# Performance work log

Hardware: AMD Instinct MI355X
Metric: run time of the kernel (lower is better)

## Reference

```python
import jax, jax.numpy as jnp
import numpy as np

DECAY = 0.8
COMMITMENT = 1.0
EPS = 1e-05


def setup_inputs() -> dict:
    key = jax.random.key(0)
    k1, k2, k3 = jax.random.split(key, 3)
    dim, n_embed = 256, 8192
    input = jax.random.normal(k1, (8, 2048, dim), dtype=jnp.float32)
    embed = jax.random.normal(k2, (dim, n_embed), dtype=jnp.float32)
    cluster_size = jnp.zeros((n_embed,), dtype=jnp.float32)
    embed_avg = jax.random.normal(k3, (dim, n_embed), dtype=jnp.float32)
    return {"input": input, "embed": embed, "cluster_size": cluster_size, "embed_avg": embed_avg}


def reference(input, embed, cluster_size, embed_avg):
    dim, n_embed = embed.shape
    flatten = input.reshape(-1, dim)  # [N, d]
    dist = (jnp.sum(flatten * flatten, axis=1, keepdims=True)
            - 2.0 * flatten @ embed
            + jnp.sum(embed * embed, axis=0, keepdims=True))  # [N, C]
    embed_ind_flat = jnp.argmin(dist, axis=1)  # [N]
    embed_ind = embed_ind_flat.reshape(input.shape[:-1])
    quantize = jnp.take(embed.T, embed_ind_flat, axis=0).reshape(input.shape)

    # training-mode EMA codebook update (onehot.sum(0) and x^T @ onehot as segment ops)
    counts = jax.ops.segment_sum(jnp.ones_like(embed_ind_flat, dtype=input.dtype),
                                 embed_ind_flat, num_segments=n_embed)  # [C]
    embed_sum = jax.ops.segment_sum(flatten, embed_ind_flat, num_segments=n_embed).T  # [d, C]
    new_cluster_size = cluster_size * DECAY + counts * (1.0 - DECAY)
    new_embed_avg = embed_avg * DECAY + embed_sum * (1.0 - DECAY)
    smoothed = (new_cluster_size + EPS) / (jnp.sum(new_cluster_size) + n_embed * EPS)
    smoothed = smoothed * jnp.sum(new_cluster_size)
    new_embed = new_embed_avg / smoothed[None, :]

    commit_loss = jnp.mean((quantize - input) ** 2) * COMMITMENT
    # straight-through (no grad here in fwd-only, values identical)
    quantize_st = input + jax.lax.stop_gradient(quantize - input)
    return quantize_st, embed_ind, commit_loss, new_embed, new_cluster_size, new_embed_avg
```

## Files before the change

### kernel.cpp

```cpp
#include <hip/hip_runtime.h>
#include <hip/hip_bf16.h>
#include <float.h>
#include <stdint.h>

#define N_ROWS 16384
#define DIM 256
#define NE 8192
#define K2 768
#define DECAY 0.8f
#define OMD 0.2f
#define EPS 1e-5f
#define NPAN 8
#define NKT 24
#define NVT 96

#define WS_X2     0
#define WS_EMBEDT 0
#define WS_ESUMT  2097152
#define WS_B2T    6291456
#define WS_ENORM  9437184
#define WS_COUNTS 9445376
#define WS_SMOOTH 9453568
#define WS_PI     9592832
#define WS_LOSS   9740288
#define WS_TOTAL  9740289

#define OUT_Q    0
#define OUT_IND  4194304
#define OUT_LOSS 4210688
#define OUT_NE   4210689
#define OUT_NCS  6307841
#define OUT_NEA  6316033

typedef __attribute__((ext_vector_type(8))) short bf16x8;
typedef __attribute__((ext_vector_type(4))) float f32x4;

static __device__ __forceinline__ ushort f2bf(float f) {
    uint32_t u = __float_as_uint(f);
    uint32_t r = (u + 0x7fffu + ((u >> 16) & 1u)) >> 16;
    return (ushort)r;
}
static __device__ __forceinline__ float bf2f(ushort h) {
    return __uint_as_float(((uint32_t)h) << 16);
}
static __device__ __forceinline__ void async16(void* lds, const void* g) {
    __builtin_amdgcn_global_load_lds(
        (const __attribute__((address_space(1))) uint32_t*)g,
        (__attribute__((address_space(3))) uint32_t*)lds, 16, 0, 0);
}

__global__ __launch_bounds__(256) void convx_kernel(const float* __restrict__ x,
                                                    ushort* __restrict__ X2) {
    int i = blockIdx.x * 256 + threadIdx.x;
    int row = i >> 6, q = (i & 63) * 4;
    float4 v = *(const float4*)&x[(size_t)row * 256 + q];
    ushort4 hi, lo;
    hi.x = f2bf(v.x); hi.y = f2bf(v.y); hi.z = f2bf(v.z); hi.w = f2bf(v.w);
    lo.x = f2bf(v.x - bf2f(hi.x)); lo.y = f2bf(v.y - bf2f(hi.y));
    lo.z = f2bf(v.z - bf2f(hi.z)); lo.w = f2bf(v.w - bf2f(hi.w));
    *(ushort4*)&X2[(size_t)row * K2 + q]       = hi;
    *(ushort4*)&X2[(size_t)row * K2 + 256 + q] = lo;
    *(ushort4*)&X2[(size_t)row * K2 + 512 + q] = hi;
}

__global__ __launch_bounds__(256) void prepB_kernel(const float* __restrict__ embed,
                                                    ushort* __restrict__ B2T,
                                                    float* __restrict__ enorm) {
    __shared__ float t[32][33];
    int c0 = blockIdx.x * 32, d0 = blockIdx.y * 32;
    int tx = threadIdx.x & 31, ty = threadIdx.x >> 5;
    #pragma unroll
    for (int r = 0; r < 4; ++r)
        t[ty + r * 8][tx] = embed[(size_t)(d0 + ty + r * 8) * NE + c0 + tx];
    __syncthreads();
    #pragma unroll
    for (int r = 0; r < 4; ++r) {
        int c = c0 + ty + r * 8, d = d0 + tx;
        float v = t[tx][ty + r * 8];
        ushort hi = f2bf(v);
        ushort lo = f2bf(v - bf2f(hi));
        B2T[(size_t)c * K2 + d]       = hi;
        B2T[(size_t)c * K2 + 256 + d] = hi;
        B2T[(size_t)c * K2 + 512 + d] = lo;
        float s = v * v;
        #pragma unroll
        for (int off = 16; off; off >>= 1) s += __shfl_down(s, off, 32);
        if (tx == 0) atomicAdd(&enorm[c], s);
    }
}

__global__ __launch_bounds__(256) void transpose_kernel(const float* __restrict__ embed,
                                                        float* __restrict__ embedT) {
    __shared__ float t[32][33];
    int c0 = blockIdx.x * 32, d0 = blockIdx.y * 32;
    int tx = threadIdx.x & 31, ty = threadIdx.x >> 5;
    #pragma unroll
    for (int r = 0; r < 4; ++r)
        t[ty + r * 8][tx] = embed[(size_t)(d0 + ty + r * 8) * NE + c0 + tx];
    __syncthreads();
    #pragma unroll
    for (int r = 0; r < 4; ++r)
        embedT[(size_t)(c0 + ty + r * 8) * DIM + d0 + tx] = t[tx][ty + r * 8];
}

#define MFMA16(d, a, b) d = __builtin_amdgcn_mfma_f32_16x16x32_bf16(a, b, d, 0, 0, 0)

__global__ __launch_bounds__(1024, 4) void argmin_mfma(
    const ushort* __restrict__ X2, const ushort* __restrict__ B2T,
    const float* __restrict__ enorm, int* __restrict__ pi) {
    __shared__ ushort smem[55296];
    float* const redv = (float*)(smem + 49152);
    int*   const redc = (int*)(smem + 51200);
    float* const enS  = (float*)(smem + 53248);

    const int lin = blockIdx.x;
    const int by = lin & 7, bx = lin >> 3;
    const int row0 = bx * 256, colb = by * 1024;

    const int tid = threadIdx.x;
    const int lane = tid & 63, wid = tid >> 6;
    const int fl = lane & 15, fh = lane >> 4;
    const int wr = wid >> 2, wc = wid & 3;

    enS[tid] = enorm[colb + tid];
    redv[tid] = FLT_MAX; redc[tid] = 0x7fffffff;

    const int srow = tid >> 2;
    const int swz = (tid & 3) ^ (srow & 3);
    const size_t aBase = (size_t)(row0 + srow) * K2 + swz * 8;
    const size_t bBase = (size_t)(colb + srow) * K2 + swz * 8;

    async16(smem + 0 * 8192 + tid * 8, X2 + aBase);
    async16(smem + 24576 + 0 * 8192 + tid * 8, B2T + bBase);
    async16(smem + 1 * 8192 + tid * 8, X2 + aBase + 32);
    async16(smem + 24576 + 1 * 8192 + tid * 8, B2T + bBase + 32);

    const int xo = (fh ^ (fl & 3)) * 8;
    int aOff[4], bOff[4];
    #pragma unroll
    for (int m = 0; m < 4; ++m) aOff[m] = (wr * 64 + m * 16 + fl) * 32 + xo;
    #pragma unroll
    for (int n = 0; n < 4; ++n) bOff[n] = (wc * 64 + n * 16 + fl) * 32 + xo;

    f32x4 acc[4][4];
    #pragma unroll
    for (int m = 0; m < 4; ++m)
        #pragma unroll
        for (int n = 0; n < 4; ++n) acc[m][n] = (f32x4){0.f, 0.f, 0.f, 0.f};

    int cur = 0;
    #pragma unroll 1
    for (int vt = 0; vt < NVT; ++vt) {
        const int t = vt % NKT;
        int nv2 = vt + 2; if (nv2 >= NVT) nv2 -= NVT;
        const int nt2 = nv2 % NKT, nct2 = nv2 / NKT;
        int nbuf = cur + 2; if (nbuf >= 3) nbuf -= 3;

        async16(smem + nbuf * 8192 + tid * 8, X2 + aBase + (size_t)nt2 * 32);
        async16(smem + 24576 + nbuf * 8192 + tid * 8,
                B2T + bBase + (size_t)nct2 * 196608 + (size_t)nt2 * 32);

        asm volatile("s_waitcnt vmcnt(4)" ::: "memory");
        __builtin_amdgcn_s_barrier();
        __builtin_amdgcn_sched_barrier(0);

        const ushort* Ac = smem + cur * 8192;
        const ushort* Bc = smem + 24576 + cur * 8192;
        bf16x8 af[4], bf[4];
        #pragma unroll
        for (int n = 0; n < 4; ++n) bf[n] = *(const bf16x8*)&Bc[bOff[n]];
        #pragma unroll
        for (int m = 0; m < 4; ++m) af[m] = *(const bf16x8*)&Ac[aOff[m]];

        __builtin_amdgcn_s_setprio(1);
        #pragma unroll
        for (int m = 0; m < 4; ++m)
            #pragma unroll
            for (int n = 0; n < 4; ++n)
                MFMA16(acc[m][n], af[m], bf[n]);
        __builtin_amdgcn_s_setprio(0);

        if (t == NKT - 1) {
            const int ct = vt / NKT;
            const int cb = colb + ct * 256 + wc * 64;
            float en[4];
            #pragma unroll
            for (int n = 0; n < 4; ++n) en[n] = enS[ct * 256 + wc * 64 + n * 16 + fl];
            #pragma unroll
            for (int m = 0; m < 4; ++m)
                #pragma unroll
                for (int r = 0; r < 4; ++r) {
                    float bv = FLT_MAX; int bc = 0x7fffffff;
                    #pragma unroll
                    for (int n = 0; n < 4; ++n) {
                        float s = __builtin_fmaf(-2.f, acc[m][n][r], en[n]);
                        int c = cb + n * 16 + fl;
                        if (s < bv) { bv = s; bc = c; }
                    }
                    #pragma unroll
                    for (int off = 1; off < 16; off <<= 1) {
                        float ov = __shfl_xor(bv, off, 64);
                        int oc = __shfl_xor(bc, off, 64);
                        if (ov < bv || (ov == bv && oc < bc)) { bv = ov; bc = oc; }
                    }
                    if (fl == 0) {
                        const int slot = (wr * 64 + m * 16 + fh * 4 + r) * 4 + wc;
                        float cv = redv[slot]; int cc = redc[slot];
                        if (bv < cv || (bv == cv && bc < cc)) {
                            redv[slot] = bv; redc[slot] = bc;
                        }
                    }
                }
            #pragma unroll
            for (int m = 0; m < 4; ++m)
                #pragma unroll
                for (int n = 0; n < 4; ++n) acc[m][n] = (f32x4){0.f, 0.f, 0.f, 0.f};
        }
        __builtin_amdgcn_s_barrier();
        __builtin_amdgcn_sched_barrier(0);
        cur = cur + 1 == 3 ? 0 : cur + 1;
    }

    asm volatile("s_waitcnt vmcnt(0) lgkmcnt(0)" ::: "memory");
    __builtin_amdgcn_s_barrier();
    if (tid < 256) {
        float bv = redv[tid * 4]; int bc = redc[tid * 4];
        #pragma unroll
        for (int w = 1; w < 4; ++w) {
            float v = redv[tid * 4 + w]; int c = redc[tid * 4 + w];
            if (v < bv || (v == bv && c < bc)) { bv = v; bc = c; }
        }
        pi[(size_t)(row0 + tid) * NPAN + by] = bc;
    }
}

__global__ __launch_bounds__(256) void rerank_gather(
    const float* __restrict__ x, const float* __restrict__ embedT,
    const int* __restrict__ pi, float* __restrict__ out_ind,
    float* __restrict__ q_out, float* __restrict__ esumT,
    float* __restrict__ counts, float* __restrict__ loss_acc) {
    const int row = blockIdx.x * 4 + (threadIdx.x >> 6);
    const int lane = threadIdx.x & 63;
    float4 xv = *(const float4*)&x[(size_t)row * DIM + lane * 4];
    float bestd = FLT_MAX; int besti = 0;
    float4 ebest = {0.f, 0.f, 0.f, 0.f};
    #pragma unroll
    for (int p = 0; p < NPAN; ++p) {
        const int c = pi[(size_t)row * NPAN + p];
        float4 e = *(const float4*)&embedT[(size_t)c * DIM + lane * 4];
        float dx = e.x - xv.x, dy = e.y - xv.y, dz = e.z - xv.z, dw = e.w - xv.w;
        float s = dx * dx + dy * dy + dz * dz + dw * dw;
        #pragma unroll
        for (int off = 32; off; off >>= 1) s += __shfl_down(s, off);
        s = __shfl(s, 0);
        if (s < bestd) { bestd = s; besti = c; ebest = e; }
    }
    *(float4*)&q_out[(size_t)row * DIM + lane * 4] = ebest;
    __shared__ float ls[4];
    if (lane == 0) {
        out_ind[row] = (float)besti;
        ls[threadIdx.x >> 6] = bestd;
        atomicAdd(&counts[besti], 1.0f);
    }
    atomicAdd(&esumT[(size_t)besti * DIM + lane * 4 + 0], xv.x);
    atomicAdd(&esumT[(size_t)besti * DIM + lane * 4 + 1], xv.y);
    atomicAdd(&esumT[(size_t)besti * DIM + lane * 4 + 2], xv.z);
    atomicAdd(&esumT[(size_t)besti * DIM + lane * 4 + 3], xv.w);
    __syncthreads();
    if (threadIdx.x == 0) atomicAdd(loss_acc, ls[0] + ls[1] + ls[2] + ls[3]);
}

__global__ void ncs_kernel(const float* __restrict__ cs, const float* __restrict__ counts,
                           float* __restrict__ out_ncs, float* __restrict__ total) {
    int c = blockIdx.x * 256 + threadIdx.x;
    float v = cs[c] * DECAY + counts[c] * OMD;
    out_ncs[c] = v;
    float s = v;
    #pragma unroll
    for (int off = 32; off; off >>= 1) s += __shfl_down(s, off);
    __shared__ float bs[4];
    if ((threadIdx.x & 63) == 0) bs[threadIdx.x >> 6] = s;
    __syncthreads();
    if (threadIdx.x == 0) atomicAdd(total, bs[0] + bs[1] + bs[2] + bs[3]);
}

__global__ void smooth_kernel(const float* __restrict__ out_ncs, const float* __restrict__ total,
                              float* __restrict__ smoothed, const float* __restrict__ loss_acc,
                              float* __restrict__ out_loss) {
    int c = blockIdx.x * 256 + threadIdx.x;
    float tot = *total;
    float v = out_ncs[c];
    smoothed[c] = (v + EPS) / (tot + (float)NE * EPS) * tot;
    if (blockIdx.x == 0 && threadIdx.x == 0)
        *out_loss = *loss_acc * (1.0f / ((float)N_ROWS * (float)DIM));
}

__global__ __launch_bounds__(256) void final_kernel(
    const float* __restrict__ embed_avg, const float* __restrict__ esumT,
    const float* __restrict__ smoothed, float* __restrict__ out_ne,
    float* __restrict__ out_nea) {
    __shared__ float t[32][33];
    int c0 = blockIdx.x * 32, d0 = blockIdx.y * 32;
    int tx = threadIdx.x & 31, ty = threadIdx.x >> 5;
    #pragma unroll
    for (int r = 0; r < 4; ++r)
        t[ty + r * 8][tx] = esumT[(size_t)(c0 + ty + r * 8) * DIM + d0 + tx];
    __syncthreads();
    #pragma unroll
    for (int r = 0; r < 4; ++r) {
        int d = d0 + ty + r * 8, c = c0 + tx;
        float es = t[tx][ty + r * 8];
        float ea = embed_avg[(size_t)d * NE + c] * DECAY + es * OMD;
        out_nea[(size_t)d * NE + c] = ea;
        out_ne[(size_t)d * NE + c] = ea / smoothed[c];
    }
}

extern "C" void kernel_launch(void* const* d_in, const int* in_sizes, int n_in,
                              void* d_out, int out_size, void* d_ws, size_t ws_size,
                              hipStream_t stream) {
    const float* input     = (const float*)d_in[0];
    const float* embed     = (const float*)d_in[1];
    const float* cs        = (const float*)d_in[2];
    const float* embed_avg = (const float*)d_in[3];
    float* out = (float*)d_out;
    float* ws  = (float*)d_ws;

    hipMemsetAsync(ws + WS_COUNTS, 0, (size_t)8192 * 4, stream);
    hipMemsetAsync(ws + WS_ENORM, 0, (size_t)8192 * 4, stream);
    hipMemsetAsync(ws + WS_LOSS, 0, (size_t)2 * 4, stream);

    convx_kernel<<<4096, 256, 0, stream>>>(input, (ushort*)(ws + WS_X2));
    prepB_kernel<<<dim3(256, 8), 256, 0, stream>>>(embed, (ushort*)(ws + WS_B2T),
                                                   ws + WS_ENORM);
    argmin_mfma<<<512, 1024, 0, stream>>>(
        (const ushort*)(ws + WS_X2), (const ushort*)(ws + WS_B2T), ws + WS_ENORM,
        (int*)(ws + WS_PI));
    transpose_kernel<<<dim3(256, 8), 256, 0, stream>>>(embed, ws + WS_EMBEDT);
    hipMemsetAsync(ws + WS_ESUMT, 0, (size_t)2097152 * 4, stream);
    rerank_gather<<<4096, 256, 0, stream>>>(input, ws + WS_EMBEDT, (int*)(ws + WS_PI),
                                            out + OUT_IND, out + OUT_Q,
                                            ws + WS_ESUMT, ws + WS_COUNTS, ws + WS_LOSS);
    ncs_kernel<<<32, 256, 0, stream>>>(cs, ws + WS_COUNTS, out + OUT_NCS, ws + WS_TOTAL);
    smooth_kernel<<<32, 256, 0, stream>>>(out + OUT_NCS, ws + WS_TOTAL, ws + WS_SMOOTH,
                                          ws + WS_LOSS, out + OUT_LOSS);
    final_kernel<<<dim3(256, 8), 256, 0, stream>>>(embed_avg, ws + WS_ESUMT, ws + WS_SMOOTH,
                                                   out + OUT_NE, out + OUT_NEA);
}
```

Baseline: 468.3 us.

## Halve argmin block to 512 threads with 128x64 per-wave MFMA tiles

The argmin GEMM kernel now runs 8 waves per block instead of 16, and each wave covers 128 rows by 64 columns with an 8x4 accumulator array. The block tile stays 256x256, so each thread issues twice as many async global-to-LDS loads, and the LDS swizzle and wait count are adjusted to match. The aim is to raise MFMA work per LDS fragment read and cut barrier and wave overhead. In exchange it roughly doubles accumulator registers and leaves fewer waves to hide latency.

```diff
diff --git a/kernel.cpp b/kernel.cpp
--- a/kernel.cpp
+++ b/kernel.cpp
@@ -105,7 +105,7 @@
 
 #define MFMA16(d, a, b) d = __builtin_amdgcn_mfma_f32_16x16x32_bf16(a, b, d, 0, 0, 0)
 
-__global__ __launch_bounds__(1024, 4) void argmin_mfma(
+__global__ __launch_bounds__(512, 2) void argmin_mfma(
     const ushort* __restrict__ X2, const ushort* __restrict__ B2T,
     const float* __restrict__ enorm, int* __restrict__ pi) {
     __shared__ ushort smem[55296];
@@ -123,28 +123,34 @@
     const int wr = wid >> 2, wc = wid & 3;
 
     enS[tid] = enorm[colb + tid];
-    redv[tid] = FLT_MAX; redc[tid] = 0x7fffffff;
+    enS[tid + 512] = enorm[colb + 512 + tid];
+    redv[tid] = FLT_MAX;       redc[tid] = 0x7fffffff;
+    redv[tid + 512] = FLT_MAX; redc[tid + 512] = 0x7fffffff;
 
     const int srow = tid >> 2;
-    const int swz = (tid & 3) ^ (srow & 3);
-    const size_t aBase = (size_t)(row0 + srow) * K2 + swz * 8;
-    const size_t bBase = (size_t)(colb + srow) * K2 + swz * 8;
-
-    async16(smem + 0 * 8192 + tid * 8, X2 + aBase);
-    async16(smem + 24576 + 0 * 8192 + tid * 8, B2T + bBase);
-    async16(smem + 1 * 8192 + tid * 8, X2 + aBase + 32);
-    async16(smem + 24576 + 1 * 8192 + tid * 8, B2T + bBase + 32);
-
-    const int xo = (fh ^ (fl & 3)) * 8;
-    int aOff[4], bOff[4];
-    #pragma unroll
-    for (int m = 0; m < 4; ++m) aOff[m] = (wr * 64 + m * 16 + fl) * 32 + xo;
+    const int swz = (tid & 3) ^ ((tid >> 4) & 3);
+    const size_t aB = (size_t)(row0 + srow) * K2 + swz * 8;
+    const size_t bB = (size_t)(colb + srow) * K2 + swz * 8;
+    const size_t jA = (size_t)128 * K2;
+
+    #pragma unroll
+    for (int tpre = 0; tpre < 2; ++tpre) {
+        async16(smem + tpre * 8192 + tid * 8, X2 + aB + (size_t)tpre * 32);
+        async16(smem + tpre * 8192 + (tid + 512) * 8, X2 + aB + jA + (size_t)tpre * 32);
+        async16(smem + 24576 + tpre * 8192 + tid * 8, B2T + bB + (size_t)tpre * 32);
+        async16(smem + 24576 + tpre * 8192 + (tid + 512) * 8, B2T + bB + jA + (size_t)tpre * 32);
+    }
+
+    const int xo = (fh ^ ((fl >> 2) & 3)) * 8;
+    int aOff[8], bOff[4];
+    #pragma unroll
+    for (int m = 0; m < 8; ++m) aOff[m] = (wr * 128 + m * 16 + fl) * 32 + xo;
     #pragma unroll
     for (int n = 0; n < 4; ++n) bOff[n] = (wc * 64 + n * 16 + fl) * 32 + xo;
 
-    f32x4 acc[4][4];
-    #pragma unroll
-    for (int m = 0; m < 4; ++m)
+    f32x4 acc[8][4];
+    #pragma unroll
+    for (int m = 0; m < 8; ++m)
         #pragma unroll
         for (int n = 0; n < 4; ++n) acc[m][n] = (f32x4){0.f, 0.f, 0.f, 0.f};
 
@@ -156,25 +162,30 @@
         const int nt2 = nv2 % NKT, nct2 = nv2 / NKT;
         int nbuf = cur + 2; if (nbuf >= 3) nbuf -= 3;
 
-        async16(smem + nbuf * 8192 + tid * 8, X2 + aBase + (size_t)nt2 * 32);
-        async16(smem + 24576 + nbuf * 8192 + tid * 8,
-                B2T + bBase + (size_t)nct2 * 196608 + (size_t)nt2 * 32);
-
-        asm volatile("s_waitcnt vmcnt(4)" ::: "memory");
+        {
+            const ushort* Xs = X2 + aB + (size_t)nt2 * 32;
+            const ushort* Bs = B2T + bB + (size_t)nct2 * 196608 + (size_t)nt2 * 32;
+            async16(smem + nbuf * 8192 + tid * 8, Xs);
+            async16(smem + nbuf * 8192 + (tid + 512) * 8, Xs + jA);
+            async16(smem + 24576 + nbuf * 8192 + tid * 8, Bs);
+            async16(smem + 24576 + nbuf * 8192 + (tid + 512) * 8, Bs + jA);
+        }
+
+        asm volatile("s_waitcnt vmcnt(8)" ::: "memory");
         __builtin_amdgcn_s_barrier();
         __builtin_amdgcn_sched_barrier(0);
 
         const ushort* Ac = smem + cur * 8192;
         const ushort* Bc = smem + 24576 + cur * 8192;
-        bf16x8 af[4], bf[4];
+        bf16x8 af[8], bf[4];
         #pragma unroll
         for (int n = 0; n < 4; ++n) bf[n] = *(const bf16x8*)&Bc[bOff[n]];
         #pragma unroll
-        for (int m = 0; m < 4; ++m) af[m] = *(const bf16x8*)&Ac[aOff[m]];
+        for (int m = 0; m < 8; ++m) af[m] = *(const bf16x8*)&Ac[aOff[m]];
 
         __builtin_amdgcn_s_setprio(1);
         #pragma unroll
-        for (int m = 0; m < 4; ++m)
+        for (int m = 0; m < 8; ++m)
             #pragma unroll
             for (int n = 0; n < 4; ++n)
                 MFMA16(acc[m][n], af[m], bf[n]);
@@ -187,7 +198,7 @@
             #pragma unroll
             for (int n = 0; n < 4; ++n) en[n] = enS[ct * 256 + wc * 64 + n * 16 + fl];
             #pragma unroll
-            for (int m = 0; m < 4; ++m)
+            for (int m = 0; m < 8; ++m)
                 #pragma unroll
                 for (int r = 0; r < 4; ++r) {
                     float bv = FLT_MAX; int bc = 0x7fffffff;
@@ -204,7 +215,7 @@
                         if (ov < bv || (ov == bv && oc < bc)) { bv = ov; bc = oc; }
                     }
                     if (fl == 0) {
-                        const int slot = (wr * 64 + m * 16 + fh * 4 + r) * 4 + wc;
+                        const int slot = (wr * 128 + m * 16 + fh * 4 + r) * 4 + wc;
                         float cv = redv[slot]; int cc = redc[slot];
                         if (bv < cv || (bv == cv && bc < cc)) {
                             redv[slot] = bv; redc[slot] = bc;
@@ -212,7 +223,7 @@
                     }
                 }
             #pragma unroll
-            for (int m = 0; m < 4; ++m)
+            for (int m = 0; m < 8; ++m)
                 #pragma unroll
                 for (int n = 0; n < 4; ++n) acc[m][n] = (f32x4){0.f, 0.f, 0.f, 0.f};
         }
@@ -333,7 +344,7 @@
     convx_kernel<<<4096, 256, 0, stream>>>(input, (ushort*)(ws + WS_X2));
     prepB_kernel<<<dim3(256, 8), 256, 0, stream>>>(embed, (ushort*)(ws + WS_B2T),
                                                    ws + WS_ENORM);
-    argmin_mfma<<<512, 1024, 0, stream>>>(
+    argmin_mfma<<<512, 512, 0, stream>>>(
         (const ushort*)(ws + WS_X2), (const ushort*)(ws + WS_B2T), ws + WS_ENORM,
         (int*)(ws + WS_PI));
     transpose_kernel<<<dim3(256, 8), 256, 0, stream>>>(embed, ws + WS_EMBEDT);
```

Result: slower. 491.8 us (+5.0%).
